# Performance work log

Measured on AMD Instinct MI355X. Metric: run time of the kernel, lower is better.

## Reference

```python
import jax, jax.numpy as jnp
import numpy as np

N = 100000          # nodes
E = 3200000         # edges (avg degree 32)
F_IN = 512
NHID = 64
NCLS = 40
ALPHA = 0.1
K = 10

def setup_inputs() -> dict:
    key = jax.random.key(0)
    ks = jax.random.split(key, 6)
    features = jax.random.normal(ks[0], (N, F_IN), dtype=jnp.float32)
    edge_index = jax.random.randint(ks[1], (2, E), 0, N)
    edge_values = jax.random.uniform(ks[2], (E,), dtype=jnp.float32)
    W1 = jax.random.normal(ks[3], (F_IN, NHID), dtype=jnp.float32) * (1.0 / np.sqrt(F_IN))
    b1 = jnp.zeros((NHID,), jnp.float32)
    W2 = jax.random.normal(ks[4], (NHID, NCLS), dtype=jnp.float32) * (1.0 / np.sqrt(NHID))
    b2 = jnp.zeros((NCLS,), jnp.float32)
    return {"features": features, "edge_index": edge_index, "edge_values": edge_values,
            "W1": W1, "b1": b1, "W2": W2, "b2": b2}

def reference(features, edge_index, edge_values, W1, b1, W2, b2):
    # eval mode: all dropouts are identity
    row, col = edge_index[0], edge_index[1]
    x = jax.nn.relu(features @ W1 + b1)       # [N, NHID]
    x = x @ W2 + b2                            # [N, NCLS]
    h = x                                      # residual (teleport) term
    def step(x, _):
        msg = edge_values[:, None] * x[col]                       # [E, NCLS]
        agg = jax.ops.segment_sum(msg, row, num_segments=N)       # spmm(adj, x)
        return (1.0 - ALPHA) * agg + ALPHA * h, None
    x, _ = jax.lax.scan(step, x, None, length=K)
    return jax.nn.log_softmax(x, axis=1)
```

## Files before the change

kernel.cpp:

```cpp
#include <hip/hip_runtime.h>
#include <hip/hip_bf16.h>

#define NN 100000
#define NE 3200000
#define F_IN 512
#define NHID 64
#define NCLS 40

#define NB2 512
#define RPB2 196
#define CHK 4096
#define NCH 782
#define EPT 16
#define ECAP 7168
#define TOT (NB2 * NCH)
#define NSB 391

#define TPN 5

#define GCOL 64
#define CSH 11
#define NBIN (RPB2 * GCOL)
#define SEG (NBIN / 256)

#define NTILE 8

__device__ __forceinline__ float bf2f(unsigned short u) {
  return __uint_as_float((unsigned)u << 16);
}
__device__ __forceinline__ unsigned short f2bf(float f) {
  unsigned u = __float_as_uint(f);
  u += 0x7FFFu + ((u >> 16) & 1u);
  return (unsigned short)(u >> 16);
}
__device__ __forceinline__ float blo(unsigned u) {
  return __uint_as_float(u << 16);
}
__device__ __forceinline__ float bhi(unsigned u) {
  return __uint_as_float(u & 0xffff0000u);
}
__device__ __forceinline__ unsigned pk(float l, float h) {
  return (unsigned)f2bf(l) | ((unsigned)f2bf(h) << 16);
}

__global__ __launch_bounds__(256) void gemm1_kernel(
    const float* __restrict__ F, const float* __restrict__ W1,
    const float* __restrict__ b1, float* __restrict__ H) {
  __shared__ float As[16][68];
  __shared__ float Bs[16][64];
  const int tid = threadIdx.x;
  const int m0 = blockIdx.x * 64;
  const int ty = tid >> 4;
  const int tx = tid & 15;
  const int lrowA = tid >> 2;
  const int lkA = (tid & 3) * 4;
  const int lkB = tid >> 4;
  const int lcolB = (tid & 15) * 4;
  const bool rowok = (m0 + lrowA) < NN;
  const int rclamp = rowok ? (m0 + lrowA) : (NN - 1);
  const float* Fb = F + (long)rclamp * F_IN + lkA;

  float acc[4][4] = {};
  for (int k0 = 0; k0 < F_IN; k0 += 16) {
    float4 fa = *(const float4*)(Fb + k0);
    if (!rowok) fa = make_float4(0.f, 0.f, 0.f, 0.f);
    float4 wb = *(const float4*)(W1 + (long)(k0 + lkB) * NHID + lcolB);
    __syncthreads();
    As[lkA + 0][lrowA] = fa.x;
    As[lkA + 1][lrowA] = fa.y;
    As[lkA + 2][lrowA] = fa.z;
    As[lkA + 3][lrowA] = fa.w;
    *(float4*)&Bs[lkB][lcolB] = wb;
    __syncthreads();
#pragma unroll
    for (int kk = 0; kk < 16; ++kk) {
      float4 a = *(const float4*)&As[kk][ty * 4];
      float4 b = *(const float4*)&Bs[kk][tx * 4];
      float av[4] = {a.x, a.y, a.z, a.w};
      float bv[4] = {b.x, b.y, b.z, b.w};
#pragma unroll
      for (int i = 0; i < 4; ++i)
#pragma unroll
        for (int j = 0; j < 4; ++j) acc[i][j] = fmaf(av[i], bv[j], acc[i][j]);
    }
  }
  float4 bb = *(const float4*)(b1 + tx * 4);
  float bv[4] = {bb.x, bb.y, bb.z, bb.w};
#pragma unroll
  for (int i = 0; i < 4; ++i) {
    int r = m0 + ty * 4 + i;
    if (r < NN) {
      float4 o;
      o.x = fmaxf(acc[i][0] + bv[0], 0.f);
      o.y = fmaxf(acc[i][1] + bv[1], 0.f);
      o.z = fmaxf(acc[i][2] + bv[2], 0.f);
      o.w = fmaxf(acc[i][3] + bv[3], 0.f);
      *(float4*)(H + (long)r * NHID + tx * 4) = o;
    }
  }
}

__global__ __launch_bounds__(256) void gemm2_kernel(
    const float* __restrict__ H, const float* __restrict__ W2,
    const float* __restrict__ b2, ushort4* __restrict__ X0b) {
  __shared__ float Ws[NHID * NCLS];
  __shared__ float bs[NCLS];
  const int tid = threadIdx.x;
  for (int i = tid; i < NHID * NCLS; i += 256) Ws[i] = W2[i];
  if (tid < NCLS) bs[tid] = b2[tid];
  __syncthreads();
  const int node = blockIdx.x * 256 + tid;
  if (node >= NN) return;
  float acc[NCLS];
#pragma unroll
  for (int j = 0; j < NCLS; ++j) acc[j] = bs[j];
  const float4* h4 = (const float4*)(H + (long)node * NHID);
#pragma unroll
  for (int kq = 0; kq < 16; ++kq) {
    float4 h = h4[kq];
    float hv[4] = {h.x, h.y, h.z, h.w};
#pragma unroll
    for (int u = 0; u < 4; ++u) {
      const int k = kq * 4 + u;
#pragma unroll
      for (int j = 0; j < NCLS; ++j)
        acc[j] = fmaf(hv[u], Ws[k * NCLS + j], acc[j]);
    }
  }
#pragma unroll
  for (int q = 0; q < 10; ++q) {
    X0b[node * 10 + q] = make_ushort4(f2bf(acc[q * 4]), f2bf(acc[q * 4 + 1]),
                                      f2bf(acc[q * 4 + 2]), f2bf(acc[q * 4 + 3]));
  }
}

__global__ __launch_bounds__(256) void p1_count(const int* __restrict__ row,
                                                int* __restrict__ hist) {
  __shared__ int h[NB2];
  const int tid = threadIdx.x, blk = blockIdx.x;
  for (int i = tid; i < NB2; i += 256) h[i] = 0;
  __syncthreads();
  const int e0 = blk * CHK;
#pragma unroll
  for (int k = 0; k < EPT; ++k) {
    int e = e0 + k * 256 + tid;
    if (e < NE) atomicAdd(&h[row[e] / RPB2], 1);
  }
  __syncthreads();
  for (int i = tid; i < NB2; i += 256) hist[blk * NB2 + i] = h[i];
}

__global__ __launch_bounds__(1024) void p2a_scan(const int* __restrict__ hist,
                                                 int* __restrict__ base,
                                                 int* __restrict__ bsum) {
  __shared__ int sm[1024];
  const int t = threadIdx.x;
  const int f = blockIdx.x * 1024 + t;
  const int b = f / NCH, blk = f - b * NCH;
  const int v = hist[blk * NB2 + b];
  sm[t] = v;
  __syncthreads();
  for (int off = 1; off < 1024; off <<= 1) {
    int u = (t >= off) ? sm[t - off] : 0;
    __syncthreads();
    sm[t] += u;
    __syncthreads();
  }
  base[f] = sm[t] - v;
  if (t == 1023) bsum[blockIdx.x] = sm[t];
}

__global__ __launch_bounds__(512) void p2b_scan(const int* __restrict__ bsum,
                                                int* __restrict__ boff) {
  __shared__ int sm[512];
  const int t = threadIdx.x;
  const int v = (t < NSB) ? bsum[t] : 0;
  sm[t] = v;
  __syncthreads();
  for (int off = 1; off < 512; off <<= 1) {
    int u = (t >= off) ? sm[t - off] : 0;
    __syncthreads();
    sm[t] += u;
    __syncthreads();
  }
  if (t < NSB) boff[t] = sm[t] - v;
}

__global__ __launch_bounds__(1024) void p2c_add(int* __restrict__ base,
                                                const int* __restrict__ boff) {
  const int f = blockIdx.x * 1024 + threadIdx.x;
  base[f] += boff[blockIdx.x];
}

__global__ __launch_bounds__(256) void p3_scatter(
    const int* __restrict__ row, const int* __restrict__ col,
    const float* __restrict__ ev, const int* __restrict__ base,
    int2* __restrict__ staged) {
  __shared__ int h[NB2], lscan[NB2], lcur[NB2], gbase[NB2];
  __shared__ int tmp[256];
  __shared__ int2 pay[CHK];
  __shared__ unsigned short binof[CHK];
  const int tid = threadIdx.x, blk = blockIdx.x;
  for (int i = tid; i < NB2; i += 256) { h[i] = 0; lcur[i] = 0; }
  __syncthreads();
  const int e0 = blk * CHK;
  const int n = (NE - e0 < CHK) ? (NE - e0) : CHK;
  int eb[EPT], em[EPT], ee[EPT];
#pragma unroll
  for (int k = 0; k < EPT; ++k) {
    int e = e0 + k * 256 + tid;
    if (e < NE) {
      int r = row[e];
      int b = r / RPB2;
      eb[k] = b;
      em[k] = (col[e] << 8) | (r - b * RPB2);
      ee[k] = __float_as_int(ev[e]);
      atomicAdd(&h[b], 1);
    } else {
      eb[k] = -1;
    }
  }
  __syncthreads();
  int a = h[2 * tid], c = h[2 * tid + 1];
  tmp[tid] = a + c;
  __syncthreads();
  for (int off = 1; off < 256; off <<= 1) {
    int v = (tid >= off) ? tmp[tid - off] : 0;
    __syncthreads();
    tmp[tid] += v;
    __syncthreads();
  }
  int excl = tmp[tid] - (a + c);
  lscan[2 * tid] = excl;
  lscan[2 * tid + 1] = excl + a;
  gbase[2 * tid] = base[(2 * tid) * NCH + blk];
  gbase[2 * tid + 1] = base[(2 * tid + 1) * NCH + blk];
  __syncthreads();
#pragma unroll
  for (int k = 0; k < EPT; ++k) {
    if (eb[k] >= 0) {
      int b = eb[k];
      int p = lscan[b] + atomicAdd(&lcur[b], 1);
      pay[p] = make_int2(em[k], ee[k]);
      binof[p] = (unsigned short)b;
    }
  }
  __syncthreads();
  for (int j = tid; j < n; j += 256) {
    int b = binof[j];
    staged[gbase[b] + (j - lscan[b])] = pay[j];
  }
}

__global__ __launch_bounds__(256) void p4_emit(
    const int* __restrict__ base, const int2* __restrict__ staged,
    int2* __restrict__ edges, int* __restrict__ rp, int* __restrict__ rp8) {
  __shared__ int bh[NBIN];
  __shared__ int tsum[256];
  __shared__ int2 pay[ECAP];
  const int b = blockIdx.x, tid = threadIdx.x;
  const int s0 = base[b * NCH];
  const int s1 = (b == NB2 - 1) ? NE : base[(b + 1) * NCH];
  const int cnt = s1 - s0;
  for (int i = tid; i < NBIN; i += 256) bh[i] = 0;
  __syncthreads();
  for (int j = tid; j < cnt; j += 256) {
    int ex = staged[s0 + j].x;
    int rl = ex & 255;
    unsigned col = (unsigned)ex >> 8;
    atomicAdd(&bh[(rl << 6) | (col >> CSH)], 1);
  }
  __syncthreads();
  int s = 0;
#pragma unroll
  for (int i = 0; i < SEG; ++i) {
    int v = bh[tid * SEG + i];
    bh[tid * SEG + i] = s;
    s += v;
  }
  tsum[tid] = s;
  __syncthreads();
  for (int off = 1; off < 256; off <<= 1) {
    int u = (tid >= off) ? tsum[tid - off] : 0;
    __syncthreads();
    tsum[tid] += u;
    __syncthreads();
  }
  const int add = (tid > 0) ? tsum[tid - 1] : 0;
#pragma unroll
  for (int i = 0; i < SEG; ++i) bh[tid * SEG + i] += add;
  __syncthreads();
  if (tid < RPB2) {
    int r = b * RPB2 + tid;
    if (r <= NN) rp[r] = s0 + bh[tid << 6];
    if (r < NN) {
#pragma unroll
      for (int t = 0; t < NTILE; ++t)
        rp8[r * NTILE + t] = s0 + bh[(tid << 6) | (t << 3)];
    }
  }
  __syncthreads();
  if (cnt <= ECAP) {
    for (int j = tid; j < cnt; j += 256) {
      int2 ed = staged[s0 + j];
      int rl = ed.x & 255;
      unsigned col = (unsigned)ed.x >> 8;
      int p = atomicAdd(&bh[(rl << 6) | (col >> CSH)], 1);
      pay[p] = make_int2((int)col, ed.y);
    }
    __syncthreads();
    for (int j = tid; j < cnt; j += 256) edges[s0 + j] = pay[j];
  } else {
    for (int j = tid; j < cnt; j += 256) {
      int2 ed = staged[s0 + j];
      int rl = ed.x & 255;
      unsigned col = (unsigned)ed.x >> 8;
      int p = atomicAdd(&bh[(rl << 6) | (col >> CSH)], 1);
      edges[s0 + p] = make_int2((int)col, ed.y);
    }
  }
}

#define FMA8(v, xb)                                              \
  a0 = fmaf(v, blo(xb.x), a0); a1 = fmaf(v, bhi(xb.x), a1);      \
  a2 = fmaf(v, blo(xb.y), a2); a3 = fmaf(v, bhi(xb.y), a3);      \
  a4 = fmaf(v, blo(xb.z), a4); a5 = fmaf(v, bhi(xb.z), a5);      \
  a6 = fmaf(v, blo(xb.w), a6); a7 = fmaf(v, bhi(xb.w), a7);

__global__ __launch_bounds__(256) void prop_kernel_bf16(
    const uint4* __restrict__ xin, uint4* __restrict__ xout,
    const uint4* __restrict__ hb, const int2* __restrict__ edges,
    const int* __restrict__ rp, const int4* __restrict__ rp8v) {
  const int t = blockIdx.x * 256 + threadIdx.x;
  const int node = t / TPN;
  if (node >= NN) return;
  const int g = t - node * TPN;
  const int e1 = rp[node + 1];
  const int4 ra = rp8v[node * 2];
  const int4 rb = rp8v[node * 2 + 1];
  int stops[NTILE];
  stops[0] = ra.y; stops[1] = ra.z; stops[2] = ra.w; stops[3] = rb.x;
  stops[4] = rb.y; stops[5] = rb.z; stops[6] = rb.w; stops[7] = e1;
  float a0 = 0.f, a1 = 0.f, a2 = 0.f, a3 = 0.f;
  float a4 = 0.f, a5 = 0.f, a6 = 0.f, a7 = 0.f;
  int e = ra.x;
#pragma unroll
  for (int tt = 0; tt < NTILE; ++tt) {
    const int estop = stops[tt];
    while (e + 4 <= estop) {
      int2 d0 = edges[e], d1 = edges[e + 1], d2 = edges[e + 2],
           d3 = edges[e + 3];
      uint4 x0 = xin[d0.x * TPN + g];
      uint4 x1 = xin[d1.x * TPN + g];
      uint4 x2 = xin[d2.x * TPN + g];
      uint4 x3 = xin[d3.x * TPN + g];
      float v0 = __int_as_float(d0.y), v1 = __int_as_float(d1.y);
      float v2 = __int_as_float(d2.y), v3 = __int_as_float(d3.y);
      FMA8(v0, x0);
      FMA8(v1, x1);
      FMA8(v2, x2);
      FMA8(v3, x3);
      e += 4;
    }
    if (e + 2 <= estop) {
      int2 d0 = edges[e], d1 = edges[e + 1];
      uint4 x0 = xin[d0.x * TPN + g];
      uint4 x1 = xin[d1.x * TPN + g];
      float v0 = __int_as_float(d0.y), v1 = __int_as_float(d1.y);
      FMA8(v0, x0);
      FMA8(v1, x1);
      e += 2;
    }
    if (e < estop) {
      int2 d0 = edges[e];
      uint4 x0 = xin[d0.x * TPN + g];
      float v0 = __int_as_float(d0.y);
      FMA8(v0, x0);
      ++e;
    }
  }
  uint4 hh = hb[node * TPN + g];
  uint4 r;
  r.x = pk(fmaf(0.9f, a0, 0.1f * blo(hh.x)), fmaf(0.9f, a1, 0.1f * bhi(hh.x)));
  r.y = pk(fmaf(0.9f, a2, 0.1f * blo(hh.y)), fmaf(0.9f, a3, 0.1f * bhi(hh.y)));
  r.z = pk(fmaf(0.9f, a4, 0.1f * blo(hh.z)), fmaf(0.9f, a5, 0.1f * bhi(hh.z)));
  r.w = pk(fmaf(0.9f, a6, 0.1f * blo(hh.w)), fmaf(0.9f, a7, 0.1f * bhi(hh.w)));
  xout[node * TPN + g] = r;
}

__global__ __launch_bounds__(256) void logsm_kernel(
    const ushort4* __restrict__ X, float* __restrict__ out) {
  const int node = blockIdx.x * 256 + threadIdx.x;
  if (node >= NN) return;
  float v[NCLS];
#pragma unroll
  for (int q = 0; q < 10; ++q) {
    ushort4 a = X[node * 10 + q];
    v[q * 4] = bf2f(a.x);
    v[q * 4 + 1] = bf2f(a.y);
    v[q * 4 + 2] = bf2f(a.z);
    v[q * 4 + 3] = bf2f(a.w);
  }
  float m = v[0];
#pragma unroll
  for (int j = 1; j < NCLS; ++j) m = fmaxf(m, v[j]);
  float s = 0.f;
#pragma unroll
  for (int j = 0; j < NCLS; ++j) s += expf(v[j] - m);
  const float l = m + logf(s);
  float4* o4 = (float4*)(out + (long)node * NCLS);
#pragma unroll
  for (int q = 0; q < 10; ++q)
    o4[q] = make_float4(v[q * 4] - l, v[q * 4 + 1] - l, v[q * 4 + 2] - l,
                        v[q * 4 + 3] - l);
}

extern "C" void kernel_launch(void* const* d_in, const int* in_sizes, int n_in,
                              void* d_out, int out_size, void* d_ws,
                              size_t ws_size, hipStream_t stream) {
  const float* F = (const float*)d_in[0];
  const int* EI = (const int*)d_in[1];
  const float* EV = (const float*)d_in[2];
  const float* W1 = (const float*)d_in[3];
  const float* b1 = (const float*)d_in[4];
  const float* W2 = (const float*)d_in[5];
  const float* b2 = (const float*)d_in[6];
  float* out = (float*)d_out;
  char* ws = (char*)d_ws;

  int2* STAGED = (int2*)(ws + 0);
  float* H = (float*)(ws + 16000000);
  int* HIST = (int*)(ws + 42000000);
  int* BASE = (int*)(ws + 43700000);
  int* BSUM = (int*)(ws + 45400000);
  int* BOFF = (int*)(ws + 45402048);
  int2* EDG = (int2*)(ws + 48000000);
  int* RP = (int*)(ws + 73600000);
  int* RP8 = (int*)(ws + 74400000);
  uint4* X0b = (uint4*)(ws + 78000000);
  uint4* XAb = (uint4*)(ws + 86400000);
  uint4* XBb = (uint4*)(ws + 94800000);

  const int* ROW = EI;
  const int* COL = EI + NE;

  p1_count<<<NCH, 256, 0, stream>>>(ROW, HIST);
  p2a_scan<<<NSB, 1024, 0, stream>>>(HIST, BASE, BSUM);
  p2b_scan<<<1, 512, 0, stream>>>(BSUM, BOFF);
  p2c_add<<<NSB, 1024, 0, stream>>>(BASE, BOFF);
  p3_scatter<<<NCH, 256, 0, stream>>>(ROW, COL, EV, BASE, STAGED);
  p4_emit<<<NB2, 256, 0, stream>>>(BASE, STAGED, EDG, RP, RP8);

  gemm1_kernel<<<(NN + 63) / 64, 256, 0, stream>>>(F, W1, b1, H);
  gemm2_kernel<<<(NN + 255) / 256, 256, 0, stream>>>(H, W2, b2,
                                                     (ushort4*)X0b);

  const int tgrid = (NN * TPN + 255) / 256;
  const uint4* cur_in = X0b;
  uint4* bufs[2] = {XAb, XBb};
  for (int it = 0; it < 10; ++it) {
    uint4* o = bufs[it & 1];
    prop_kernel_bf16<<<tgrid, 256, 0, stream>>>(cur_in, o, X0b, EDG, RP,
                                                (const int4*)RP8);
    cur_in = o;
  }
  logsm_kernel<<<(NN + 255) / 256, 256, 0, stream>>>((const ushort4*)cur_in,
                                                     out);
}
```

Baseline: 964.1 us.

## Fuse propagation iterations and log-softmax into one cooperative persistent kernel

Replaces the ten separate propagation launches and the log-softmax launch with a single cooperative kernel that uses grid-wide syncs between iterations and grid-stride loops over node/group work. Node rows are padded to a stride of 8 uint4 (128 bytes) instead of 5, so each node's features line up with cache lines. This removes kernel launch gaps and tail effects, at the cost of grid.sync overhead and a fixed grid size that may lower occupancy or load balance. The padding raises memory footprint and shifts the buffer offsets.

```diff
diff --git a/kernel.cpp b/kernel.cpp
--- a/kernel.cpp
+++ b/kernel.cpp
@@ -1,5 +1,8 @@
 #include <hip/hip_runtime.h>
 #include <hip/hip_bf16.h>
+#include <hip/hip_cooperative_groups.h>
+
+namespace cg = cooperative_groups;
 
 #define NN 100000
 #define NE 3200000
@@ -17,6 +20,7 @@
 #define NSB 391
 
 #define TPN 5
+#define XSTR 8
 
 #define GCOL 64
 #define CSH 11
@@ -129,7 +133,7 @@
   }
 #pragma unroll
   for (int q = 0; q < 10; ++q) {
-    X0b[node * 10 + q] = make_ushort4(f2bf(acc[q * 4]), f2bf(acc[q * 4 + 1]),
+    X0b[node * 16 + q] = make_ushort4(f2bf(acc[q * 4]), f2bf(acc[q * 4 + 1]),
                                       f2bf(acc[q * 4 + 2]), f2bf(acc[q * 4 + 3]));
   }
 }
@@ -327,92 +331,96 @@
   a4 = fmaf(v, blo(xb.z), a4); a5 = fmaf(v, bhi(xb.z), a5);      \
   a6 = fmaf(v, blo(xb.w), a6); a7 = fmaf(v, bhi(xb.w), a7);
 
-__global__ __launch_bounds__(256) void prop_kernel_bf16(
-    const uint4* __restrict__ xin, uint4* __restrict__ xout,
-    const uint4* __restrict__ hb, const int2* __restrict__ edges,
-    const int* __restrict__ rp, const int4* __restrict__ rp8v) {
-  const int t = blockIdx.x * 256 + threadIdx.x;
-  const int node = t / TPN;
-  if (node >= NN) return;
-  const int g = t - node * TPN;
-  const int e1 = rp[node + 1];
-  const int4 ra = rp8v[node * 2];
-  const int4 rb = rp8v[node * 2 + 1];
-  int stops[NTILE];
-  stops[0] = ra.y; stops[1] = ra.z; stops[2] = ra.w; stops[3] = rb.x;
-  stops[4] = rb.y; stops[5] = rb.z; stops[6] = rb.w; stops[7] = e1;
-  float a0 = 0.f, a1 = 0.f, a2 = 0.f, a3 = 0.f;
-  float a4 = 0.f, a5 = 0.f, a6 = 0.f, a7 = 0.f;
-  int e = ra.x;
-#pragma unroll
-  for (int tt = 0; tt < NTILE; ++tt) {
-    const int estop = stops[tt];
-    while (e + 4 <= estop) {
-      int2 d0 = edges[e], d1 = edges[e + 1], d2 = edges[e + 2],
-           d3 = edges[e + 3];
-      uint4 x0 = xin[d0.x * TPN + g];
-      uint4 x1 = xin[d1.x * TPN + g];
-      uint4 x2 = xin[d2.x * TPN + g];
-      uint4 x3 = xin[d3.x * TPN + g];
-      float v0 = __int_as_float(d0.y), v1 = __int_as_float(d1.y);
-      float v2 = __int_as_float(d2.y), v3 = __int_as_float(d3.y);
-      FMA8(v0, x0);
-      FMA8(v1, x1);
-      FMA8(v2, x2);
-      FMA8(v3, x3);
-      e += 4;
-    }
-    if (e + 2 <= estop) {
-      int2 d0 = edges[e], d1 = edges[e + 1];
-      uint4 x0 = xin[d0.x * TPN + g];
-      uint4 x1 = xin[d1.x * TPN + g];
-      float v0 = __int_as_float(d0.y), v1 = __int_as_float(d1.y);
-      FMA8(v0, x0);
-      FMA8(v1, x1);
-      e += 2;
-    }
-    if (e < estop) {
-      int2 d0 = edges[e];
-      uint4 x0 = xin[d0.x * TPN + g];
-      float v0 = __int_as_float(d0.y);
-      FMA8(v0, x0);
-      ++e;
-    }
-  }
-  uint4 hh = hb[node * TPN + g];
-  uint4 r;
-  r.x = pk(fmaf(0.9f, a0, 0.1f * blo(hh.x)), fmaf(0.9f, a1, 0.1f * bhi(hh.x)));
-  r.y = pk(fmaf(0.9f, a2, 0.1f * blo(hh.y)), fmaf(0.9f, a3, 0.1f * bhi(hh.y)));
-  r.z = pk(fmaf(0.9f, a4, 0.1f * blo(hh.z)), fmaf(0.9f, a5, 0.1f * bhi(hh.z)));
-  r.w = pk(fmaf(0.9f, a6, 0.1f * blo(hh.w)), fmaf(0.9f, a7, 0.1f * bhi(hh.w)));
-  xout[node * TPN + g] = r;
-}
-
-__global__ __launch_bounds__(256) void logsm_kernel(
-    const ushort4* __restrict__ X, float* __restrict__ out) {
-  const int node = blockIdx.x * 256 + threadIdx.x;
-  if (node >= NN) return;
-  float v[NCLS];
-#pragma unroll
-  for (int q = 0; q < 10; ++q) {
-    ushort4 a = X[node * 10 + q];
-    v[q * 4] = bf2f(a.x);
-    v[q * 4 + 1] = bf2f(a.y);
-    v[q * 4 + 2] = bf2f(a.z);
-    v[q * 4 + 3] = bf2f(a.w);
-  }
-  float m = v[0];
-#pragma unroll
-  for (int j = 1; j < NCLS; ++j) m = fmaxf(m, v[j]);
-  float s = 0.f;
-#pragma unroll
-  for (int j = 0; j < NCLS; ++j) s += expf(v[j] - m);
-  const float l = m + logf(s);
-  float4* o4 = (float4*)(out + (long)node * NCLS);
-#pragma unroll
-  for (int q = 0; q < 10; ++q)
-    o4[q] = make_float4(v[q * 4] - l, v[q * 4 + 1] - l, v[q * 4 + 2] - l,
-                        v[q * 4 + 3] - l);
+__global__ __launch_bounds__(256, 8) void prop_fused(
+    const uint4* __restrict__ x0, uint4* __restrict__ xa,
+    uint4* __restrict__ xb, const int2* __restrict__ edges,
+    const int4* __restrict__ rp8v, const int* __restrict__ rp,
+    float* __restrict__ out) {
+  cg::grid_group grid = cg::this_grid();
+  const int gsize = gridDim.x * 256;
+  const int gtid = blockIdx.x * 256 + threadIdx.x;
+  const uint4* in = x0;
+
+  for (int it = 0; it < 10; ++it) {
+    uint4* o = (it & 1) ? xb : xa;
+    for (int t = gtid; t < NN * TPN; t += gsize) {
+      const int node = t / TPN;
+      const int g = t - node * TPN;
+      const int4 ra = rp8v[node * 2];
+      const int4 rb = rp8v[node * 2 + 1];
+      const int e1 = rp[node + 1];
+      int stops[NTILE];
+      stops[0] = ra.y; stops[1] = ra.z; stops[2] = ra.w; stops[3] = rb.x;
+      stops[4] = rb.y; stops[5] = rb.z; stops[6] = rb.w; stops[7] = e1;
+      float a0 = 0.f, a1 = 0.f, a2 = 0.f, a3 = 0.f;
+      float a4 = 0.f, a5 = 0.f, a6 = 0.f, a7 = 0.f;
+      int e = ra.x;
+#pragma unroll
+      for (int tt = 0; tt < NTILE; ++tt) {
+        const int estop = stops[tt];
+        while (e + 4 <= estop) {
+          int2 d0 = edges[e], d1 = edges[e + 1], d2 = edges[e + 2],
+               d3 = edges[e + 3];
+          uint4 x0v = in[d0.x * XSTR + g];
+          uint4 x1v = in[d1.x * XSTR + g];
+          uint4 x2v = in[d2.x * XSTR + g];
+          uint4 x3v = in[d3.x * XSTR + g];
+          float v0 = __int_as_float(d0.y), v1 = __int_as_float(d1.y);
+          float v2 = __int_as_float(d2.y), v3 = __int_as_float(d3.y);
+          FMA8(v0, x0v);
+          FMA8(v1, x1v);
+          FMA8(v2, x2v);
+          FMA8(v3, x3v);
+          e += 4;
+        }
+        while (e < estop) {
+          int2 d0 = edges[e];
+          uint4 xv = in[d0.x * XSTR + g];
+          float v0 = __int_as_float(d0.y);
+          FMA8(v0, xv);
+          ++e;
+        }
+      }
+      uint4 hh = x0[node * XSTR + g];
+      uint4 r;
+      r.x = pk(fmaf(0.9f, a0, 0.1f * blo(hh.x)),
+               fmaf(0.9f, a1, 0.1f * bhi(hh.x)));
+      r.y = pk(fmaf(0.9f, a2, 0.1f * blo(hh.y)),
+               fmaf(0.9f, a3, 0.1f * bhi(hh.y)));
+      r.z = pk(fmaf(0.9f, a4, 0.1f * blo(hh.z)),
+               fmaf(0.9f, a5, 0.1f * bhi(hh.z)));
+      r.w = pk(fmaf(0.9f, a6, 0.1f * blo(hh.w)),
+               fmaf(0.9f, a7, 0.1f * bhi(hh.w)));
+      o[node * XSTR + g] = r;
+    }
+    grid.sync();
+    in = o;
+  }
+
+  const ushort4* X = (const ushort4*)in;
+  for (int node = gtid; node < NN; node += gsize) {
+    float v[NCLS];
+#pragma unroll
+    for (int q = 0; q < 10; ++q) {
+      ushort4 a = X[node * 16 + q];
+      v[q * 4] = bf2f(a.x);
+      v[q * 4 + 1] = bf2f(a.y);
+      v[q * 4 + 2] = bf2f(a.z);
+      v[q * 4 + 3] = bf2f(a.w);
+    }
+    float m = v[0];
+#pragma unroll
+    for (int j = 1; j < NCLS; ++j) m = fmaxf(m, v[j]);
+    float s = 0.f;
+#pragma unroll
+    for (int j = 0; j < NCLS; ++j) s += expf(v[j] - m);
+    const float l = m + logf(s);
+    float4* o4 = (float4*)(out + (long)node * NCLS);
+#pragma unroll
+    for (int q = 0; q < 10; ++q)
+      o4[q] = make_float4(v[q * 4] - l, v[q * 4 + 1] - l, v[q * 4 + 2] - l,
+                          v[q * 4 + 3] - l);
+  }
 }
 
 extern "C" void kernel_launch(void* const* d_in, const int* in_sizes, int n_in,
@@ -438,8 +446,8 @@
   int* RP = (int*)(ws + 73600000);
   int* RP8 = (int*)(ws + 74400000);
   uint4* X0b = (uint4*)(ws + 78000000);
-  uint4* XAb = (uint4*)(ws + 86400000);
-  uint4* XBb = (uint4*)(ws + 94800000);
+  uint4* XAb = (uint4*)(ws + 91000000);
+  uint4* XBb = (uint4*)(ws + 104000000);
 
   const int* ROW = EI;
   const int* COL = EI + NE;
@@ -455,15 +463,16 @@
   gemm2_kernel<<<(NN + 255) / 256, 256, 0, stream>>>(H, W2, b2,
                                                      (ushort4*)X0b);
 
-  const int tgrid = (NN * TPN + 255) / 256;
-  const uint4* cur_in = X0b;
-  uint4* bufs[2] = {XAb, XBb};
-  for (int it = 0; it < 10; ++it) {
-    uint4* o = bufs[it & 1];
-    prop_kernel_bf16<<<tgrid, 256, 0, stream>>>(cur_in, o, X0b, EDG, RP,
-                                                (const int4*)RP8);
-    cur_in = o;
-  }
-  logsm_kernel<<<(NN + 255) / 256, 256, 0, stream>>>((const ushort4*)cur_in,
-                                                     out);
-}
+  {
+    int bpc = 0;
+    hipOccupancyMaxActiveBlocksPerMultiprocessor(&bpc, prop_fused, 256, 0);
+    if (bpc < 1) bpc = 1;
+    if (bpc > 8) bpc = 8;
+    const int nblk = bpc * 256;
+    const uint4* x0c = X0b;
+    void* args[] = {(void*)&x0c, (void*)&XAb, (void*)&XBb,
+                    (void*)&EDG, (void*)&RP8, (void*)&RP, (void*)&out};
+    hipLaunchCooperativeKernel(reinterpret_cast<void*>(prop_fused),
+                               dim3(nblk), dim3(256), args, 0, stream);
+  }
+}
```

Result: slower. 2.402 ms (+149.2%).
